# Kernel optimization log

Hardware: AMD Instinct MI355X
Metric: run time of the kernel (lower is better)

Reference implementation:

```python
import jax, jax.numpy as jnp
import numpy as np

B = 8192
N_CLASSES = 10

_AX = 'abcd'
_CNOT = jnp.array([[1, 0, 0, 0], [0, 1, 0, 0], [0, 0, 0, 1], [0, 0, 1, 0]], jnp.float32).reshape(2, 2, 2, 2)


def _ry(theta):
    c, s = jnp.cos(theta / 2), jnp.sin(theta / 2)
    return jnp.stack([jnp.stack([c, -s]), jnp.stack([s, c])])  # [2,2]


def _ap1(state, U, w):
    # apply single-qubit gate U on wire w; state: [N,2,2,2,2]
    i = _AX[:w] + 'i' + _AX[w + 1:]
    o = _AX[:w] + 'o' + _AX[w + 1:]
    return jnp.einsum(f'oi,n{i}->n{o}', U, state)


def _ap2(state, U, w0, w1):
    # apply two-qubit gate U [2,2,2,2]=(out0,out1,in0,in1) on wires (w0,w1)
    i, o = list(_AX), list(_AX)
    i[w0], i[w1] = 'i', 'j'
    o[w0], o[w1] = 'o', 'p'
    return jnp.einsum(f"opij,n{''.join(i)}->n{''.join(o)}", U, state)


def quantum_features(data, q_params):
    # data: [N,4] RY encoding angles applied to |0000>
    h = data / 2
    v = jnp.stack([jnp.cos(h), jnp.sin(h)], -1)  # [N,4,2]
    state = jnp.einsum('na,nb,nc,nd->nabcd', v[:, 0], v[:, 1], v[:, 2], v[:, 3])
    # fixed 8-op random layer instance (real-valued): 5 RY + 3 CNOT
    state = _ap1(state, _ry(q_params[0]), 0)
    state = _ap1(state, _ry(q_params[1]), 1)
    state = _ap2(state, _CNOT, 0, 1)
    state = _ap1(state, _ry(q_params[2]), 2)
    state = _ap1(state, _ry(q_params[3]), 3)
    state = _ap2(state, _CNOT, 2, 3)
    state = _ap1(state, _ry(q_params[4]), 1)
    state = _ap2(state, _CNOT, 1, 2)
    probs = state * state  # real statevector -> |amp|^2
    sgn = jnp.array([1.0, -1.0], jnp.float32)
    z = jnp.stack([
        jnp.einsum('nabcd,a->n', probs, sgn),
        jnp.einsum('nabcd,b->n', probs, sgn),
        jnp.einsum('nabcd,c->n', probs, sgn),
        jnp.einsum('nabcd,d->n', probs, sgn)], -1)
    return z  # [N,4] PauliZ expectations


def setup_inputs() -> dict:
    key = jax.random.key(0)
    ks = jax.random.split(key, 6)
    return {
        'x': jax.random.normal(ks[0], (B, 1, 28, 28), jnp.float32),
        'conv_w': jax.random.normal(ks[1], (4, 1, 2, 2), jnp.float32) * 0.5,
        'conv_b': jax.random.normal(ks[2], (4,), jnp.float32) * 0.1,
        'q_params': jax.random.uniform(ks[3], (5,), jnp.float32, 0.0, 2.0 * np.pi),
        'lin_w': jax.random.normal(ks[4], (N_CLASSES, 1568), jnp.float32) * 0.02,
        'lin_b': jnp.zeros((N_CLASSES,), jnp.float32),
    }


def reference(x, conv_w, conv_b, q_params, lin_w, lin_b):
    feats = jax.lax.conv_general_dilated(
        x, conv_w, window_strides=(2, 2), padding='VALID',
        dimension_numbers=('NCHW', 'OIHW', 'NCHW')) + conv_b[None, :, None, None]
    bsz = feats.shape[0]
    flat = feats.reshape(bsz, -1)  # [B,784]
    # extractor views flat as [B,28,28] and takes 2x2 patches -> [B*196,4]
    patches = flat.reshape(bsz, 14, 2, 14, 2).transpose(0, 1, 3, 2, 4).reshape(bsz * 196, 4)
    q = quantum_features(patches, q_params).reshape(bsz, 784)
    combined = jnp.concatenate([flat, q], axis=1)  # [B,1568]
    logits = combined @ lin_w.T + lin_b
    return jax.nn.log_softmax(logits, axis=-1)
```

## Files before the change

kernel.cpp:

```cpp
#include <hip/hip_runtime.h>
#include <hip/hip_bf16.h>


#define SPB 4
#define THREADS 256
#define NCLS 10
#define FEAT 1568

__global__ __launch_bounds__(THREADS, 6)
void quanv_fused_kernel(const float* __restrict__ x,
                        const float* __restrict__ conv_w,
                        const float* __restrict__ conv_b,
                        const float* __restrict__ q_params,
                        const float* __restrict__ lin_w,
                        const float* __restrict__ lin_b,
                        float* __restrict__ out)
{
    __shared__ float comb[SPB][FEAT];
    __shared__ float part[SPB][2][12];

    const int tid = threadIdx.x;
    const int n0  = blockIdx.x * SPB;

    float W[4][4], Bc[4];
    #pragma unroll
    for (int c = 0; c < 4; ++c) {
        #pragma unroll
        for (int k = 0; k < 4; ++k) W[c][k] = conv_w[c * 4 + k];
        Bc[c] = conv_b[c];
    }
    const float qp0 = q_params[0], qp1 = q_params[1];
    const float qp2 = q_params[2], qp3 = q_params[3];
    const float q4  = q_params[4];
    const float cq4 = __cosf(q4), sq4 = __sinf(q4);

    for (int p = tid; p < SPB * 14 * 7; p += THREADS) {
        const int s = p / 98, t = p % 98;
        const int h = t / 7, wp = t % 7;
        const float* xp = x + (size_t)(n0 + s) * 784 + 56 * h + 4 * wp;
        const float4 r0 = *reinterpret_cast<const float4*>(xp);
        const float4 r1 = *reinterpret_cast<const float4*>(xp + 28);
        const int r = h * 14 + 2 * wp;
        #pragma unroll
        for (int c = 0; c < 4; ++c) {
            comb[s][c * 196 + r] =
                fmaf(r0.x, W[c][0], fmaf(r0.y, W[c][1],
                fmaf(r1.x, W[c][2], fmaf(r1.y, W[c][3], Bc[c]))));
            comb[s][c * 196 + r + 1] =
                fmaf(r0.z, W[c][0], fmaf(r0.w, W[c][1],
                fmaf(r1.z, W[c][2], fmaf(r1.w, W[c][3], Bc[c]))));
        }
    }
    __syncthreads();

    for (int p = tid; p < SPB * 196; p += THREADS) {
        const int s = p / 196, r = p % 196;
        const int i = r / 14, j = r % 14;
        const int base = 56 * i + 2 * j;
        const float2 d01 = *reinterpret_cast<const float2*>(&comb[s][base]);
        const float2 d23 = *reinterpret_cast<const float2*>(&comb[s][base + 28]);
        const float a0 = d01.x + qp0, a1 = d01.y + qp1;
        const float a2 = d23.x + qp2, a3 = d23.y + qp3;
        const float c0 = __cosf(a0);
        const float c1 = __cosf(a1), s1 = __sinf(a1);
        const float c2 = __cosf(a2), c3 = __cosf(a3);
        const float z0 = c0;
        const float z1 = cq4 * c0 * c1 - sq4 * s1;
        const float z2 = z1 * c2;
        const float z3 = c2 * c3;
        *reinterpret_cast<float4*>(&comb[s][784 + r * 4]) =
            make_float4(z0, z1, z2, z3);
    }
    __syncthreads();

    const int wave = tid >> 6, lane = tid & 63;
    const int pr = wave & 1;
    const int h  = wave >> 1;
    const int s0 = 2 * pr, s1 = s0 + 1;
    const int kbase = h * 784;

    float acc0[NCLS], acc1[NCLS];
    #pragma unroll
    for (int c = 0; c < NCLS; ++c) { acc0[c] = 0.f; acc1[c] = 0.f; }

    #pragma unroll
    for (int kb = 0; kb < 3; ++kb) {
        const int k = kbase + kb * 256 + lane * 4;
        const float4 v0 = *reinterpret_cast<const float4*>(&comb[s0][k]);
        const float4 v1 = *reinterpret_cast<const float4*>(&comb[s1][k]);
        #pragma unroll
        for (int c = 0; c < NCLS; ++c) {
            const float4 w4 = *reinterpret_cast<const float4*>(&lin_w[c * FEAT + k]);
            acc0[c] = fmaf(v0.x, w4.x, fmaf(v0.y, w4.y,
                      fmaf(v0.z, w4.z, fmaf(v0.w, w4.w, acc0[c]))));
            acc1[c] = fmaf(v1.x, w4.x, fmaf(v1.y, w4.y,
                      fmaf(v1.z, w4.z, fmaf(v1.w, w4.w, acc1[c]))));
        }
    }
    if (lane < 16) {
        const int k = kbase + 768 + lane;
        const float v0 = comb[s0][k];
        const float v1 = comb[s1][k];
        #pragma unroll
        for (int c = 0; c < NCLS; ++c) {
            const float w = lin_w[c * FEAT + k];
            acc0[c] = fmaf(v0, w, acc0[c]);
            acc1[c] = fmaf(v1, w, acc1[c]);
        }
    }

    #pragma unroll
    for (int m = 1; m < 64; m <<= 1) {
        #pragma unroll
        for (int c = 0; c < NCLS; ++c) {
            acc0[c] += __shfl_xor(acc0[c], m, 64);
            acc1[c] += __shfl_xor(acc1[c], m, 64);
        }
    }

    if (lane == 0) {
        #pragma unroll
        for (int c = 0; c < NCLS; ++c) {
            part[s0][h][c] = acc0[c];
            part[s1][h][c] = acc1[c];
        }
    }
    __syncthreads();

    if (tid < SPB) {
        const int s = tid;
        float lg[NCLS], mx = -1e30f;
        #pragma unroll
        for (int c = 0; c < NCLS; ++c) {
            lg[c] = part[s][0][c] + part[s][1][c] + lin_b[c];
            mx = fmaxf(mx, lg[c]);
        }
        float sum = 0.f;
        #pragma unroll
        for (int c = 0; c < NCLS; ++c) sum += __expf(lg[c] - mx);
        const float lse = mx + __logf(sum);
        float* o = out + (size_t)(n0 + s) * NCLS;
        #pragma unroll
        for (int c = 0; c < NCLS; ++c) o[c] = lg[c] - lse;
    }
}

extern "C" void kernel_launch(void* const* d_in, const int* in_sizes, int n_in,
                              void* d_out, int out_size, void* d_ws, size_t ws_size,
                              hipStream_t stream) {
    const float* x        = (const float*)d_in[0];
    const float* conv_w   = (const float*)d_in[1];
    const float* conv_b   = (const float*)d_in[2];
    const float* q_params = (const float*)d_in[3];
    const float* lin_w    = (const float*)d_in[4];
    const float* lin_b    = (const float*)d_in[5];
    float* out = (float*)d_out;

    const int B = in_sizes[0] / 784;
    const int nblocks = B / SPB;

    quanv_fused_kernel<<<nblocks, THREADS, 0, stream>>>(
        x, conv_w, conv_b, q_params, lin_w, lin_b, out);
}
```

Measured before the change: 101.1 us.

## Fuse quantum feature computation into the linear dot product and double samples per block

The quantum features are now computed in registers inside the linear-layer loop, so the second shared-memory stage and its barrier are gone. Shared memory holds only the conv output. Each block now processes 8 samples, so every wave accumulates 4 samples per lin_w load, which halves weight reloads per sample. The cost is a larger register footprint (40 accumulators), a lower occupancy hint, and divergent work between half-waves: waves on the quantum half do trig while waves on the flat half only load.

```diff
diff --git a/kernel.cpp b/kernel.cpp
--- a/kernel.cpp
+++ b/kernel.cpp
@@ -2,12 +2,13 @@
 #include <hip/hip_bf16.h>
 
 
-#define SPB 4
+#define SPB 8
 #define THREADS 256
 #define NCLS 10
 #define FEAT 1568
+#define HALF 784
 
-__global__ __launch_bounds__(THREADS, 6)
+__global__ __launch_bounds__(THREADS, 4)
 void quanv_fused_kernel(const float* __restrict__ x,
                         const float* __restrict__ conv_w,
                         const float* __restrict__ conv_b,
@@ -16,7 +17,7 @@
                         const float* __restrict__ lin_b,
                         float* __restrict__ out)
 {
-    __shared__ float comb[SPB][FEAT];
+    __shared__ __attribute__((aligned(16))) float flat[SPB][HALF];
     __shared__ float part[SPB][2][12];
 
     const int tid = threadIdx.x;
@@ -34,7 +35,7 @@
     const float q4  = q_params[4];
     const float cq4 = __cosf(q4), sq4 = __sinf(q4);
 
-    for (int p = tid; p < SPB * 14 * 7; p += THREADS) {
+    for (int p = tid; p < SPB * 98; p += THREADS) {
         const int s = p / 98, t = p % 98;
         const int h = t / 7, wp = t % 7;
         const float* xp = x + (size_t)(n0 + s) * 784 + 56 * h + 4 * wp;
@@ -43,87 +44,119 @@
         const int r = h * 14 + 2 * wp;
         #pragma unroll
         for (int c = 0; c < 4; ++c) {
-            comb[s][c * 196 + r] =
+            const float v0 =
                 fmaf(r0.x, W[c][0], fmaf(r0.y, W[c][1],
                 fmaf(r1.x, W[c][2], fmaf(r1.y, W[c][3], Bc[c]))));
-            comb[s][c * 196 + r + 1] =
+            const float v1 =
                 fmaf(r0.z, W[c][0], fmaf(r0.w, W[c][1],
                 fmaf(r1.z, W[c][2], fmaf(r1.w, W[c][3], Bc[c]))));
+            *reinterpret_cast<float2*>(&flat[s][c * 196 + r]) =
+                make_float2(v0, v1);
         }
     }
     __syncthreads();
 
-    for (int p = tid; p < SPB * 196; p += THREADS) {
-        const int s = p / 196, r = p % 196;
-        const int i = r / 14, j = r % 14;
-        const int base = 56 * i + 2 * j;
-        const float2 d01 = *reinterpret_cast<const float2*>(&comb[s][base]);
-        const float2 d23 = *reinterpret_cast<const float2*>(&comb[s][base + 28]);
-        const float a0 = d01.x + qp0, a1 = d01.y + qp1;
-        const float a2 = d23.x + qp2, a3 = d23.y + qp3;
-        const float c0 = __cosf(a0);
-        const float c1 = __cosf(a1), s1 = __sinf(a1);
-        const float c2 = __cosf(a2), c3 = __cosf(a3);
-        const float z0 = c0;
-        const float z1 = cq4 * c0 * c1 - sq4 * s1;
-        const float z2 = z1 * c2;
-        const float z3 = c2 * c3;
-        *reinterpret_cast<float4*>(&comb[s][784 + r * 4]) =
-            make_float4(z0, z1, z2, z3);
-    }
-    __syncthreads();
+    const int wave = tid >> 6, lane = tid & 63;
+    const int hh = wave & 1, pb = wave >> 1;
+    const int sm0 = 2 * pb, sm1 = sm0 + 1, sm2 = sm0 + 4, sm3 = sm0 + 5;
+    const int kbase = hh * HALF;
 
-    const int wave = tid >> 6, lane = tid & 63;
-    const int pr = wave & 1;
-    const int h  = wave >> 1;
-    const int s0 = 2 * pr, s1 = s0 + 1;
-    const int kbase = h * 784;
-
-    float acc0[NCLS], acc1[NCLS];
+    float acc[4][NCLS];
     #pragma unroll
-    for (int c = 0; c < NCLS; ++c) { acc0[c] = 0.f; acc1[c] = 0.f; }
+    for (int m = 0; m < 4; ++m)
+        #pragma unroll
+        for (int c = 0; c < NCLS; ++c) acc[m][c] = 0.f;
 
     #pragma unroll
     for (int kb = 0; kb < 3; ++kb) {
         const int k = kbase + kb * 256 + lane * 4;
-        const float4 v0 = *reinterpret_cast<const float4*>(&comb[s0][k]);
-        const float4 v1 = *reinterpret_cast<const float4*>(&comb[s1][k]);
+        float4 v[4];
+        if (hh == 0) {
+            const int kk = kb * 256 + lane * 4;
+            v[0] = *reinterpret_cast<const float4*>(&flat[sm0][kk]);
+            v[1] = *reinterpret_cast<const float4*>(&flat[sm1][kk]);
+            v[2] = *reinterpret_cast<const float4*>(&flat[sm2][kk]);
+            v[3] = *reinterpret_cast<const float4*>(&flat[sm3][kk]);
+        } else {
+            const int r = kb * 64 + lane;
+            const int i = r / 14, j = r - 14 * i;
+            const int f0 = 56 * i + 2 * j;
+            const int sms[4] = {sm0, sm1, sm2, sm3};
+            #pragma unroll
+            for (int m = 0; m < 4; ++m) {
+                const float2 d01 = *reinterpret_cast<const float2*>(&flat[sms[m]][f0]);
+                const float2 d23 = *reinterpret_cast<const float2*>(&flat[sms[m]][f0 + 28]);
+                const float a0 = d01.x + qp0, a1 = d01.y + qp1;
+                const float a2 = d23.x + qp2, a3 = d23.y + qp3;
+                const float c0 = __cosf(a0);
+                const float c1 = __cosf(a1), s1 = __sinf(a1);
+                const float c2 = __cosf(a2), c3 = __cosf(a3);
+                const float z1 = cq4 * c0 * c1 - sq4 * s1;
+                v[m] = make_float4(c0, z1, z1 * c2, c2 * c3);
+            }
+        }
         #pragma unroll
         for (int c = 0; c < NCLS; ++c) {
             const float4 w4 = *reinterpret_cast<const float4*>(&lin_w[c * FEAT + k]);
-            acc0[c] = fmaf(v0.x, w4.x, fmaf(v0.y, w4.y,
-                      fmaf(v0.z, w4.z, fmaf(v0.w, w4.w, acc0[c]))));
-            acc1[c] = fmaf(v1.x, w4.x, fmaf(v1.y, w4.y,
-                      fmaf(v1.z, w4.z, fmaf(v1.w, w4.w, acc1[c]))));
+            #pragma unroll
+            for (int m = 0; m < 4; ++m) {
+                acc[m][c] = fmaf(v[m].x, w4.x, fmaf(v[m].y, w4.y,
+                            fmaf(v[m].z, w4.z, fmaf(v[m].w, w4.w, acc[m][c]))));
+            }
         }
     }
+
     if (lane < 16) {
         const int k = kbase + 768 + lane;
-        const float v0 = comb[s0][k];
-        const float v1 = comb[s1][k];
+        float vv[4];
+        if (hh == 0) {
+            const int kk = 768 + lane;
+            vv[0] = flat[sm0][kk]; vv[1] = flat[sm1][kk];
+            vv[2] = flat[sm2][kk]; vv[3] = flat[sm3][kk];
+        } else {
+            const int r = 192 + (lane >> 2);
+            const int e = lane & 3;
+            const int i = r / 14, j = r - 14 * i;
+            const int f0 = 56 * i + 2 * j;
+            const int sms[4] = {sm0, sm1, sm2, sm3};
+            #pragma unroll
+            for (int m = 0; m < 4; ++m) {
+                const float2 d01 = *reinterpret_cast<const float2*>(&flat[sms[m]][f0]);
+                const float2 d23 = *reinterpret_cast<const float2*>(&flat[sms[m]][f0 + 28]);
+                const float a0 = d01.x + qp0, a1 = d01.y + qp1;
+                const float a2 = d23.x + qp2, a3 = d23.y + qp3;
+                const float c0 = __cosf(a0);
+                const float c1 = __cosf(a1), s1 = __sinf(a1);
+                const float c2 = __cosf(a2), c3 = __cosf(a3);
+                const float z1 = cq4 * c0 * c1 - sq4 * s1;
+                const float z2 = z1 * c2, z3 = c2 * c3;
+                vv[m] = (e == 0) ? c0 : ((e == 1) ? z1 : ((e == 2) ? z2 : z3));
+            }
+        }
         #pragma unroll
         for (int c = 0; c < NCLS; ++c) {
             const float w = lin_w[c * FEAT + k];
-            acc0[c] = fmaf(v0, w, acc0[c]);
-            acc1[c] = fmaf(v1, w, acc1[c]);
+            #pragma unroll
+            for (int m = 0; m < 4; ++m) acc[m][c] = fmaf(vv[m], w, acc[m][c]);
         }
     }
 
     #pragma unroll
-    for (int m = 1; m < 64; m <<= 1) {
+    for (int msk = 1; msk < 64; msk <<= 1) {
         #pragma unroll
-        for (int c = 0; c < NCLS; ++c) {
-            acc0[c] += __shfl_xor(acc0[c], m, 64);
-            acc1[c] += __shfl_xor(acc1[c], m, 64);
-        }
+        for (int m = 0; m < 4; ++m)
+            #pragma unroll
+            for (int c = 0; c < NCLS; ++c)
+                acc[m][c] += __shfl_xor(acc[m][c], msk, 64);
     }
 
     if (lane == 0) {
+        const int sms[4] = {sm0, sm1, sm2, sm3};
         #pragma unroll
-        for (int c = 0; c < NCLS; ++c) {
-            part[s0][h][c] = acc0[c];
-            part[s1][h][c] = acc1[c];
-        }
+        for (int m = 0; m < 4; ++m)
+            #pragma unroll
+            for (int c = 0; c < NCLS; ++c)
+                part[sms[m]][hh][c] = acc[m][c];
     }
     __syncthreads();
 
```

After: 107.4 us. 1.06x slower.
